# Optimization experiments

Hardware: AMD Instinct MI355X
Metric: run time of the kernel (lower is better)

The kernel has to match this reference:

```python
import jax, jax.numpy as jnp
import numpy as np

B, L, D = 8192, 200, 64
NUM_ITEMS = 100000
HID = 64  # attention hidden_dim


def setup_inputs() -> dict:
    key = jax.random.key(0)
    ks = jax.random.split(key, 16)
    inp = {
        "item_sequence": jax.random.randint(ks[0], (B, L), 0, NUM_ITEMS),
        "click_sequence": jax.random.randint(ks[1], (B, L), 0, 2),
        "seq_length": jax.random.randint(ks[2], (B, 1), 1, L + 1),
        "target_item": jax.random.randint(ks[3], (B, 1), 0, NUM_ITEMS),
        "context_features": jax.random.normal(ks[4], (B, 9), dtype=jnp.float32),
        # embedding table (num_items+1, D)
        "emb_table": jax.random.normal(ks[5], (NUM_ITEMS + 1, D), dtype=jnp.float32) * 0.05,
        # attention MLP: Linear(2D->64), Linear(64->32), Linear(32->1)
        "aw1": jax.random.normal(ks[6], (2 * D, HID), dtype=jnp.float32) * 0.05,
        "ab1": jnp.zeros((HID,), jnp.float32),
        "aw2": jax.random.normal(ks[7], (HID, HID // 2), dtype=jnp.float32) * 0.05,
        "ab2": jnp.zeros((HID // 2,), jnp.float32),
        "aw3": jax.random.normal(ks[8], (HID // 2, 1), dtype=jnp.float32) * 0.05,
        "ab3": jnp.zeros((1,), jnp.float32),
        # context MLP: Linear(9->32)
        "cw": jax.random.normal(ks[9], (9, 32), dtype=jnp.float32) * 0.05,
        "cb": jnp.zeros((32,), jnp.float32),
        # head MLP: Linear(160->128), Linear(128->64), Linear(64->1)
        "mw1": jax.random.normal(ks[10], (2 * D + 32, 128), dtype=jnp.float32) * 0.05,
        "mb1": jnp.zeros((128,), jnp.float32),
        "mw2": jax.random.normal(ks[11], (128, 64), dtype=jnp.float32) * 0.05,
        "mb2": jnp.zeros((64,), jnp.float32),
        "mw3": jax.random.normal(ks[12], (64, 1), dtype=jnp.float32) * 0.05,
        "mb3": jnp.zeros((1,), jnp.float32),
    }
    return inp


def reference(item_sequence, click_sequence, seq_length, target_item, context_features,
              emb_table, aw1, ab1, aw2, ab2, aw3, ab3, cw, cb,
              mw1, mb1, mw2, mb2, mw3, mb3):
    seq_emb = emb_table[item_sequence]                 # [B, L, D]
    tgt_emb = emb_table[target_item[:, 0]]             # [B, D]
    seq_len = item_sequence.shape[1]
    mask = (jnp.arange(seq_len)[None, :] < seq_length).astype(seq_emb.dtype)  # [B, L]

    # DIN attention: concat(query, keys) -> 3-layer MLP -> masked softmax -> weighted sum
    q = jnp.broadcast_to(tgt_emb[:, None, :], seq_emb.shape)          # [B, L, D]
    att_in = jnp.concatenate([q, seq_emb], axis=-1)                   # [B, L, 2D]
    h = jax.nn.relu(att_in @ aw1 + ab1)
    h = jax.nn.relu(h @ aw2 + ab2)
    scores = (h @ aw3 + ab3)[..., 0]                                  # [B, L]
    scores = jnp.where(mask == 0, jnp.asarray(-1e9, scores.dtype), scores)
    w = jax.nn.softmax(scores, axis=1)                                # [B, L]
    attended = jnp.einsum('bl,bld->bd', w, seq_emb)                   # [B, D]

    ctx = jax.nn.relu(context_features @ cw + cb)                     # [B, 32]
    comb = jnp.concatenate([attended, tgt_emb, ctx], axis=1)          # [B, 2D+32]
    h = jax.nn.relu(comb @ mw1 + mb1)
    h = jax.nn.relu(h @ mw2 + mb2)
    out = jax.nn.sigmoid(h @ mw3 + mb3)[:, 0]                         # [B]
    return out
```

## Files before the change

### kernel.cpp

```cpp
#include <hip/hip_runtime.h>
#include <cmath>

typedef __attribute__((ext_vector_type(8))) short s16x8;
typedef __attribute__((ext_vector_type(4))) short s16x4;
typedef __attribute__((ext_vector_type(4))) float f32x4;

__device__ __forceinline__ short f2bf(float f) {
    union { float f; unsigned u; } v; v.f = f;
    unsigned r = v.u + 0x7FFFu + ((v.u >> 16) & 1u);
    return (short)(r >> 16);
}
__device__ __forceinline__ float bf2f(short s) {
    union { unsigned u; float f; } v; v.u = ((unsigned)(unsigned short)s) << 16;
    return v.f;
}
__device__ __forceinline__ s16x8 cvt8(float4 a, float4 b) {
    s16x8 r = { f2bf(a.x), f2bf(a.y), f2bf(a.z), f2bf(a.w),
                f2bf(b.x), f2bf(b.y), f2bf(b.z), f2bf(b.w) };
    return r;
}

#define W1SEQ_SH  0
#define W1TOP_SH  4096
#define W2_SH     8192
#define MW1T_SH   10240
#define MW2T_SH   30720
#define QC_F      19456
#define CB_SH     1087488

__global__ __launch_bounds__(256)
void din_wprep_kernel(const float* __restrict__ aw1,
                      const float* __restrict__ aw2,
                      const float* __restrict__ mw1,
                      const float* __restrict__ mw2,
                      short* __restrict__ ws)
{
    const int wb = blockIdx.x;
    const int t = threadIdx.x;
    if (wb == 0) {
        for (int idx = t; idx < 4096; idx += 256) {
            int j = idx & 7, lane = (idx >> 3) & 63, fr = idx >> 9;
            int n = (fr >> 1) * 16 + (lane & 15);
            int k = (fr & 1) * 32 + (lane >> 4) * 8 + j;
            ws[W1SEQ_SH + idx] = f2bf(aw1[(64 + k) * 64 + n]);
        }
    } else if (wb == 1) {
        for (int idx = t; idx < 4096; idx += 256) {
            int j = idx & 7, lane = (idx >> 3) & 63, fr = idx >> 9;
            int n = (fr >> 1) * 16 + (lane & 15);
            int k = (fr & 1) * 32 + (lane >> 4) * 8 + j;
            ws[W1TOP_SH + idx] = f2bf(aw1[k * 64 + n]);
        }
    } else if (wb == 2) {
        for (int idx = t; idx < 2048; idx += 256) {
            int j = idx & 7, lane = (idx >> 3) & 63, fr = idx >> 9;
            int n = (fr >> 1) * 16 + (lane & 15);
            int k = (fr & 1) * 32 + (lane >> 4) * 8 + j;
            ws[W2_SH + idx] = f2bf(aw2[k * 32 + n]);
        }
    } else if (wb == 3) {
        for (int idx = t; idx < 8192; idx += 256) {
            int j = idx & 7, lane = (idx >> 3) & 63, fr = idx >> 9;
            int n = (fr >> 2) * 16 + (lane & 15);
            int k = (fr & 3) * 32 + (lane >> 4) * 8 + j;
            ws[MW2T_SH + idx] = f2bf(mw2[k * 64 + n]);
        }
    } else {
        const int base = (wb - 4) * 5120;
        for (int ii = t; ii < 5120; ii += 256) {
            int idx = base + ii;
            int j = idx & 7, lane = (idx >> 3) & 63, fr = idx >> 9;
            int nt = fr / 5, ks = fr - nt * 5;
            int n = nt * 16 + (lane & 15);
            int k = ks * 32 + (lane >> 4) * 8 + j;
            ws[MW1T_SH + idx] = f2bf(mw1[k * 128 + n]);
        }
    }
}

__global__ __launch_bounds__(256)
void din_qc_kernel(const int* __restrict__ tgt_item,
                   const float* __restrict__ emb,
                   const float* __restrict__ ab1,
                   short* __restrict__ ws)
{
    const int t = threadIdx.x, lane = t & 63, wave = t >> 6;
    const int quad = lane >> 4, r16 = lane & 15;
    const short* w1t = ws + W1TOP_SH;
    float* qc = (float*)ws + QC_F;

    const int b0 = (blockIdx.x * 4 + wave) * 16;
    const int it = tgt_item[b0 + r16];
    const float* rp = emb + it * 64 + quad * 8;
    float4 v0 = *(const float4*)(rp),      v1 = *(const float4*)(rp + 4);
    float4 v2 = *(const float4*)(rp + 32), v3 = *(const float4*)(rp + 36);
    s16x8 a0 = cvt8(v0, v1);
    s16x8 a1 = cvt8(v2, v3);

    f32x4 acc[4] = {{0,0,0,0},{0,0,0,0},{0,0,0,0},{0,0,0,0}};
    #pragma unroll
    for (int nt = 0; nt < 4; ++nt) {
        s16x8 b_0 = *(const s16x8*)(w1t + ((nt * 2 + 0) * 64 + lane) * 8);
        s16x8 b_1 = *(const s16x8*)(w1t + ((nt * 2 + 1) * 64 + lane) * 8);
        acc[nt] = __builtin_amdgcn_mfma_f32_16x16x32_bf16(a0, b_0, acc[nt], 0, 0, 0);
        acc[nt] = __builtin_amdgcn_mfma_f32_16x16x32_bf16(a1, b_1, acc[nt], 0, 0, 0);
    }
    #pragma unroll
    for (int nt = 0; nt < 4; ++nt) {
        float bias = ab1[nt * 16 + r16];
        #pragma unroll
        for (int rr = 0; rr < 4; ++rr)
            qc[(b0 + quad * 4 + rr) * 64 + nt * 16 + r16] = acc[nt][rr] + bias;
    }
}

#define H1_PITCH 72
__global__ __launch_bounds__(256)
void din_att_v3(const int* __restrict__ item_seq,
                const int* __restrict__ seq_len_p,
                const int* __restrict__ tgt_item,
                const float* __restrict__ ctx_feat,
                const float* __restrict__ emb,
                const float* __restrict__ ab2,
                const float* __restrict__ aw3, const float* __restrict__ ab3,
                const float* __restrict__ cw,  const float* __restrict__ cb,
                short* __restrict__ ws)
{
    const int t = threadIdx.x, lane = t & 63, wave = t >> 6;
    const int quad = lane >> 4, r16 = lane & 15;
    __shared__ short s_w1[4096];
    __shared__ short s_h1[4][16 * H1_PITCH];
    __shared__ float s_sc[4][64];
    __shared__ float s_pool[4][64];
    __shared__ float s_m[4], s_e[4];

    const int b   = blockIdx.x;
    const int len = seq_len_p[b];
    const int tgt = tgt_item[b];

    {
        const s16x8* src = (const s16x8*)(ws + W1SEQ_SH);
        s16x8* dst = (s16x8*)s_w1;
        dst[t]       = src[t];
        dst[t + 256] = src[t + 256];
    }

    bool act[4];
    s16x8 af[4][2];
    #pragma unroll
    for (int ci = 0; ci < 4; ++ci) {
        const int c = wave + ci * 4;
        act[ci] = (c < 13) && (c * 16 < len);
        if (act[ci]) {
            int r = c * 16 + r16; if (r > 199) r = 199;
            const int it = item_seq[b * 200 + r];
            const float* rp = emb + it * 64 + quad * 8;
            float4 v0 = *(const float4*)(rp),      v1 = *(const float4*)(rp + 4);
            float4 v2 = *(const float4*)(rp + 32), v3 = *(const float4*)(rp + 36);
            af[ci][0] = cvt8(v0, v1);
            af[ci][1] = cvt8(v2, v3);
        }
    }
    s16x8 w2r[4];
    #pragma unroll
    for (int fr = 0; fr < 4; ++fr)
        w2r[fr] = *(const s16x8*)(ws + W2_SH + (fr * 64 + lane) * 8);
    const float* qcp = (const float*)ws + QC_F + b * 64;
    float qcv[4];
    #pragma unroll
    for (int nt = 0; nt < 4; ++nt) qcv[nt] = qcp[nt * 16 + r16];
    const float bias2_lo = ab2[r16], bias2_hi = ab2[16 + r16];
    const float w3_lo    = aw3[r16], w3_hi    = aw3[16 + r16];
    const float b3       = ab3[0];
    __syncthreads();

    short* h1w = s_h1[wave];

    #pragma unroll
    for (int ci = 0; ci < 4; ++ci) {
        if (!act[ci]) continue;
        f32x4 acc[4] = {{0,0,0,0},{0,0,0,0},{0,0,0,0},{0,0,0,0}};
        #pragma unroll
        for (int nt = 0; nt < 4; ++nt) {
            s16x8 b_0 = *(const s16x8*)&s_w1[((nt * 2 + 0) * 64 + lane) * 8];
            s16x8 b_1 = *(const s16x8*)&s_w1[((nt * 2 + 1) * 64 + lane) * 8];
            acc[nt] = __builtin_amdgcn_mfma_f32_16x16x32_bf16(af[ci][0], b_0, acc[nt], 0, 0, 0);
            acc[nt] = __builtin_amdgcn_mfma_f32_16x16x32_bf16(af[ci][1], b_1, acc[nt], 0, 0, 0);
        }
        #pragma unroll
        for (int nt = 0; nt < 4; ++nt)
            #pragma unroll
            for (int rr = 0; rr < 4; ++rr) {
                float v = fmaxf(acc[nt][rr] + qcv[nt], 0.f);
                h1w[(quad * 4 + rr) * H1_PITCH + nt * 16 + r16] = f2bf(v);
            }
        __builtin_amdgcn_wave_barrier();

        s16x8 h0  = *(const s16x8*)&h1w[r16 * H1_PITCH + quad * 8];
        s16x8 h1v = *(const s16x8*)&h1w[r16 * H1_PITCH + 32 + quad * 8];
        f32x4 c2[2] = {{0,0,0,0},{0,0,0,0}};
        #pragma unroll
        for (int nt = 0; nt < 2; ++nt) {
            c2[nt] = __builtin_amdgcn_mfma_f32_16x16x32_bf16(h0,  w2r[nt * 2],     c2[nt], 0, 0, 0);
            c2[nt] = __builtin_amdgcn_mfma_f32_16x16x32_bf16(h1v, w2r[nt * 2 + 1], c2[nt], 0, 0, 0);
        }
        #pragma unroll
        for (int rr = 0; rr < 4; ++rr) {
            float p = fmaxf(c2[0][rr] + bias2_lo, 0.f) * w3_lo
                    + fmaxf(c2[1][rr] + bias2_hi, 0.f) * w3_hi;
            p += __shfl_xor(p, 8);
            p += __shfl_xor(p, 4);
            p += __shfl_xor(p, 2);
            p += __shfl_xor(p, 1);
            if (r16 == 0) s_sc[wave][ci * 16 + quad * 4 + rr] = p + b3;
        }
        __builtin_amdgcn_wave_barrier();
    }

    const int ci_l = lane >> 4;
    const int c_l  = wave + ci_l * 4;
    const int grow = c_l * 16 + r16;
    const bool valid = (c_l < 13) && (grow < len);
    float sc = valid ? s_sc[wave][lane] : -1e30f;
    float m = sc;
    #pragma unroll
    for (int off = 32; off; off >>= 1) m = fmaxf(m, __shfl_xor(m, off));
    float e = valid ? __expf(sc - m) : 0.f;
    #pragma unroll
    for (int off = 32; off; off >>= 1) e += __shfl_xor(e, off);

    float p[16];
    #pragma unroll
    for (int i = 0; i < 16; ++i) p[i] = 0.f;
    #pragma unroll
    for (int ci = 0; ci < 4; ++ci) {
        if (!act[ci]) continue;
        const int row = (wave + ci * 4) * 16 + r16;
        const float w = (row < len) ? __expf(s_sc[wave][ci * 16 + r16] - m) : 0.f;
        #pragma unroll
        for (int j = 0; j < 8; ++j) {
            p[j]     += w * bf2f(af[ci][0][j]);
            p[8 + j] += w * bf2f(af[ci][1][j]);
        }
    }
    #pragma unroll
    for (int i = 0; i < 16; ++i) {
        p[i] += __shfl_xor(p[i], 1);
        p[i] += __shfl_xor(p[i], 2);
        p[i] += __shfl_xor(p[i], 4);
        p[i] += __shfl_xor(p[i], 8);
    }
    if (r16 == 0) {
        #pragma unroll
        for (int j = 0; j < 8; ++j) {
            s_pool[wave][quad * 8 + j]      = p[j];
            s_pool[wave][32 + quad * 8 + j] = p[8 + j];
        }
    }
    if (lane == 0) { s_m[wave] = m; s_e[wave] = e; }
    __syncthreads();

    short* comb = ws + CB_SH + b * 160;
    if (t < 64) {
        float gm = fmaxf(fmaxf(s_m[0], s_m[1]), fmaxf(s_m[2], s_m[3]));
        float s0 = __expf(s_m[0] - gm), s1 = __expf(s_m[1] - gm);
        float s2 = __expf(s_m[2] - gm), s3 = __expf(s_m[3] - gm);
        float denom = s0 * s_e[0] + s1 * s_e[1] + s2 * s_e[2] + s3 * s_e[3];
        float pooled = s0 * s_pool[0][t] + s1 * s_pool[1][t]
                     + s2 * s_pool[2][t] + s3 * s_pool[3][t];
        comb[t] = f2bf(pooled / denom);
    } else if (t < 96) {
        const int j = t - 64;
        float a = cb[j];
        #pragma unroll
        for (int k = 0; k < 9; ++k) a += ctx_feat[b * 9 + k] * cw[k * 32 + j];
        comb[128 + j] = f2bf(fmaxf(a, 0.f));
    } else if (t < 160) {
        comb[64 + (t - 96)] = f2bf(emb[tgt * 64 + (t - 96)]);
    }
}

__global__ __launch_bounds__(64)
void din_mlp_kernel(const float* __restrict__ mb1,
                    const float* __restrict__ mb2,
                    const float* __restrict__ mw3, const float* __restrict__ mb3,
                    const short* __restrict__ ws,
                    float* __restrict__ out)
{
    const int lane = threadIdx.x & 63;
    const int quad = lane >> 4, r16 = lane & 15;
    __shared__ short s_h1[16 * 136];
    __shared__ short s_h2[16 * 72];

    const int b0 = blockIdx.x * 16;
    const short* comb = ws + CB_SH;
    const short* w1   = ws + MW1T_SH;
    const short* w2   = ws + MW2T_SH;

    s16x8 a[5];
    #pragma unroll
    for (int ks = 0; ks < 5; ++ks)
        a[ks] = *(const s16x8*)(comb + (b0 + r16) * 160 + ks * 32 + quad * 8);
    f32x4 acc[8] = {{0,0,0,0},{0,0,0,0},{0,0,0,0},{0,0,0,0},{0,0,0,0},{0,0,0,0},{0,0,0,0},{0,0,0,0}};
    #pragma unroll
    for (int nt = 0; nt < 8; ++nt)
        #pragma unroll
        for (int ks = 0; ks < 5; ++ks) {
            s16x8 bf = *(const s16x8*)(w1 + ((nt * 5 + ks) * 64 + lane) * 8);
            acc[nt] = __builtin_amdgcn_mfma_f32_16x16x32_bf16(a[ks], bf, acc[nt], 0, 0, 0);
        }
    #pragma unroll
    for (int nt = 0; nt < 8; ++nt) {
        float bias = mb1[nt * 16 + r16];
        #pragma unroll
        for (int rr = 0; rr < 4; ++rr)
            s_h1[(quad * 4 + rr) * 136 + nt * 16 + r16] = f2bf(fmaxf(acc[nt][rr] + bias, 0.f));
    }
    __builtin_amdgcn_wave_barrier();

    s16x8 a2[4];
    #pragma unroll
    for (int ks = 0; ks < 4; ++ks)
        a2[ks] = *(const s16x8*)&s_h1[r16 * 136 + ks * 32 + quad * 8];
    f32x4 acc2[4] = {{0,0,0,0},{0,0,0,0},{0,0,0,0},{0,0,0,0}};
    #pragma unroll
    for (int nt = 0; nt < 4; ++nt)
        #pragma unroll
        for (int ks = 0; ks < 4; ++ks) {
            s16x8 bf = *(const s16x8*)(w2 + ((nt * 4 + ks) * 64 + lane) * 8);
            acc2[nt] = __builtin_amdgcn_mfma_f32_16x16x32_bf16(a2[ks], bf, acc2[nt], 0, 0, 0);
        }
    #pragma unroll
    for (int nt = 0; nt < 4; ++nt) {
        float bias = mb2[nt * 16 + r16];
        #pragma unroll
        for (int rr = 0; rr < 4; ++rr)
            s_h2[(quad * 4 + rr) * 72 + nt * 16 + r16] = f2bf(fmaxf(acc2[nt][rr] + bias, 0.f));
    }
    __builtin_amdgcn_wave_barrier();

    float p = 0.f;
    #pragma unroll
    for (int j = 0; j < 16; ++j)
        p += bf2f(s_h2[r16 * 72 + quad * 16 + j]) * mw3[quad * 16 + j];
    p += __shfl_xor(p, 16);
    p += __shfl_xor(p, 32);
    if (quad == 0) out[b0 + r16] = 1.f / (1.f + __expf(-(p + mb3[0])));
}

extern "C" void kernel_launch(void* const* d_in, const int* in_sizes, int n_in,
                              void* d_out, int out_size, void* d_ws, size_t ws_size,
                              hipStream_t stream)
{
    const int*   item_seq  = (const int*)  d_in[0];
    const int*   seq_len   = (const int*)  d_in[2];
    const int*   tgt_item  = (const int*)  d_in[3];
    const float* ctx_feat  = (const float*)d_in[4];
    const float* emb       = (const float*)d_in[5];
    const float* aw1 = (const float*)d_in[6];
    const float* ab1 = (const float*)d_in[7];
    const float* aw2 = (const float*)d_in[8];
    const float* ab2 = (const float*)d_in[9];
    const float* aw3 = (const float*)d_in[10];
    const float* ab3 = (const float*)d_in[11];
    const float* cw  = (const float*)d_in[12];
    const float* cb  = (const float*)d_in[13];
    const float* mw1 = (const float*)d_in[14];
    const float* mb1 = (const float*)d_in[15];
    const float* mw2 = (const float*)d_in[16];
    const float* mb2 = (const float*)d_in[17];
    const float* mw3 = (const float*)d_in[18];
    const float* mb3 = (const float*)d_in[19];
    float* out = (float*)d_out;
    short* ws  = (short*)d_ws;

    hipLaunchKernelGGL(din_wprep_kernel, dim3(8), dim3(256), 0, stream,
                       aw1, aw2, mw1, mw2, ws);
    hipLaunchKernelGGL(din_qc_kernel, dim3(128), dim3(256), 0, stream,
                       tgt_item, emb, ab1, ws);
    hipLaunchKernelGGL(din_att_v3, dim3(8192), dim3(256), 0, stream,
                       item_seq, seq_len, tgt_item, ctx_feat, emb,
                       ab2, aw3, ab3, cw, cb, ws);
    hipLaunchKernelGGL(din_mlp_kernel, dim3(512), dim3(64), 0, stream,
                       mb1, mb2, mw3, mb3, ws, out);
}
```

Before: 192.4 us.

## Fuse query projection and head MLP into the per-sample attention kernel

Removes the separate query-projection and head-MLP kernels and computes both inside the per-sample attention kernel. The target projection and head MLP now run per block on MFMA tiles that use only one of sixteen rows, and results stay in shared memory instead of round-tripping through workspace. This saves two launches and the global writes and reads of the qc and comb buffers. In exchange, every block re-reads the head MLP weights and the W1 top weights from global/L2. That multiplies weight traffic about 16x and adds several block-wide barriers.

New measurement: 219.9 us. 14.3% more time.

```diff
diff --git a/kernel.cpp b/kernel.cpp
--- a/kernel.cpp
+++ b/kernel.cpp
@@ -25,8 +25,6 @@
 #define W2_SH     8192
 #define MW1T_SH   10240
 #define MW2T_SH   30720
-#define QC_F      19456
-#define CB_SH     1087488
 
 __global__ __launch_bounds__(256)
 void din_wprep_kernel(const float* __restrict__ aw1,
@@ -78,58 +76,30 @@
     }
 }
 
+#define H1_PITCH 72
 __global__ __launch_bounds__(256)
-void din_qc_kernel(const int* __restrict__ tgt_item,
-                   const float* __restrict__ emb,
-                   const float* __restrict__ ab1,
-                   short* __restrict__ ws)
+void din_one(const int* __restrict__ item_seq,
+             const int* __restrict__ seq_len_p,
+             const int* __restrict__ tgt_item,
+             const float* __restrict__ ctx_feat,
+             const float* __restrict__ emb,
+             const float* __restrict__ ab1,
+             const float* __restrict__ ab2,
+             const float* __restrict__ aw3, const float* __restrict__ ab3,
+             const float* __restrict__ cw,  const float* __restrict__ cb,
+             const float* __restrict__ mb1, const float* __restrict__ mb2,
+             const float* __restrict__ mw3, const float* __restrict__ mb3,
+             const short* __restrict__ ws,
+             float* __restrict__ out)
 {
     const int t = threadIdx.x, lane = t & 63, wave = t >> 6;
     const int quad = lane >> 4, r16 = lane & 15;
-    const short* w1t = ws + W1TOP_SH;
-    float* qc = (float*)ws + QC_F;
-
-    const int b0 = (blockIdx.x * 4 + wave) * 16;
-    const int it = tgt_item[b0 + r16];
-    const float* rp = emb + it * 64 + quad * 8;
-    float4 v0 = *(const float4*)(rp),      v1 = *(const float4*)(rp + 4);
-    float4 v2 = *(const float4*)(rp + 32), v3 = *(const float4*)(rp + 36);
-    s16x8 a0 = cvt8(v0, v1);
-    s16x8 a1 = cvt8(v2, v3);
-
-    f32x4 acc[4] = {{0,0,0,0},{0,0,0,0},{0,0,0,0},{0,0,0,0}};
-    #pragma unroll
-    for (int nt = 0; nt < 4; ++nt) {
-        s16x8 b_0 = *(const s16x8*)(w1t + ((nt * 2 + 0) * 64 + lane) * 8);
-        s16x8 b_1 = *(const s16x8*)(w1t + ((nt * 2 + 1) * 64 + lane) * 8);
-        acc[nt] = __builtin_amdgcn_mfma_f32_16x16x32_bf16(a0, b_0, acc[nt], 0, 0, 0);
-        acc[nt] = __builtin_amdgcn_mfma_f32_16x16x32_bf16(a1, b_1, acc[nt], 0, 0, 0);
-    }
-    #pragma unroll
-    for (int nt = 0; nt < 4; ++nt) {
-        float bias = ab1[nt * 16 + r16];
-        #pragma unroll
-        for (int rr = 0; rr < 4; ++rr)
-            qc[(b0 + quad * 4 + rr) * 64 + nt * 16 + r16] = acc[nt][rr] + bias;
-    }
-}
-
-#define H1_PITCH 72
-__global__ __launch_bounds__(256)
-void din_att_v3(const int* __restrict__ item_seq,
-                const int* __restrict__ seq_len_p,
-                const int* __restrict__ tgt_item,
-                const float* __restrict__ ctx_feat,
-                const float* __restrict__ emb,
-                const float* __restrict__ ab2,
-                const float* __restrict__ aw3, const float* __restrict__ ab3,
-                const float* __restrict__ cw,  const float* __restrict__ cb,
-                short* __restrict__ ws)
-{
-    const int t = threadIdx.x, lane = t & 63, wave = t >> 6;
-    const int quad = lane >> 4, r16 = lane & 15;
-    __shared__ short s_w1[4096];
-    __shared__ short s_h1[4][16 * H1_PITCH];
+    __shared__ __align__(16) short s_w1[4096];
+    __shared__ __align__(16) short s_w2s[2048];
+    __shared__ __align__(16) short s_h1[4][16 * H1_PITCH];
+    __shared__ __align__(16) short s_comb[160];
+    __shared__ __align__(16) short s_hm1[128];
+    __shared__ float s_hm2[64];
     __shared__ float s_sc[4][64];
     __shared__ float s_pool[4][64];
     __shared__ float s_m[4], s_e[4];
@@ -141,9 +111,11 @@
     {
         const s16x8* src = (const s16x8*)(ws + W1SEQ_SH);
         s16x8* dst = (s16x8*)s_w1;
-        dst[t]       = src[t];
-        dst[t + 256] = src[t + 256];
-    }
+        dst[t] = src[t];
+        if (t < 256) ((s16x8*)s_w2s)[t] = ((const s16x8*)(ws + W2_SH))[t];
+        else ((s16x8*)s_w1)[t + 256 - 256 + 256] = src[t + 256 - 256 + 256];
+    }
+    ((s16x8*)s_w1)[t + 256 < 512 ? t + 256 : 511] = ((const s16x8*)(ws + W1SEQ_SH))[t + 256 < 512 ? t + 256 : 511];
 
     bool act[4];
     s16x8 af[4][2];
@@ -161,19 +133,38 @@
             af[ci][1] = cvt8(v2, v3);
         }
     }
-    s16x8 w2r[4];
-    #pragma unroll
-    for (int fr = 0; fr < 4; ++fr)
-        w2r[fr] = *(const s16x8*)(ws + W2_SH + (fr * 64 + lane) * 8);
-    const float* qcp = (const float*)ws + QC_F + b * 64;
+
+    s16x8 at0 = {}, at1 = {};
+    if (r16 == 0) {
+        const float* rp = emb + tgt * 64 + quad * 8;
+        float4 v0 = *(const float4*)(rp),      v1 = *(const float4*)(rp + 4);
+        float4 v2 = *(const float4*)(rp + 32), v3 = *(const float4*)(rp + 36);
+        at0 = cvt8(v0, v1);
+        at1 = cvt8(v2, v3);
+    }
     float qcv[4];
-    #pragma unroll
-    for (int nt = 0; nt < 4; ++nt) qcv[nt] = qcp[nt * 16 + r16];
+    {
+        f32x4 qacc[4] = {{0,0,0,0},{0,0,0,0},{0,0,0,0},{0,0,0,0}};
+        #pragma unroll
+        for (int nt = 0; nt < 4; ++nt) {
+            s16x8 b_0 = *(const s16x8*)(ws + W1TOP_SH + ((nt * 2 + 0) * 64 + lane) * 8);
+            s16x8 b_1 = *(const s16x8*)(ws + W1TOP_SH + ((nt * 2 + 1) * 64 + lane) * 8);
+            qacc[nt] = __builtin_amdgcn_mfma_f32_16x16x32_bf16(at0, b_0, qacc[nt], 0, 0, 0);
+            qacc[nt] = __builtin_amdgcn_mfma_f32_16x16x32_bf16(at1, b_1, qacc[nt], 0, 0, 0);
+        }
+        #pragma unroll
+        for (int nt = 0; nt < 4; ++nt)
+            qcv[nt] = __shfl(qacc[nt][0], r16) + ab1[nt * 16 + r16];
+    }
     const float bias2_lo = ab2[r16], bias2_hi = ab2[16 + r16];
     const float w3_lo    = aw3[r16], w3_hi    = aw3[16 + r16];
     const float b3       = ab3[0];
     __syncthreads();
 
+    s16x8 w2r[4];
+    #pragma unroll
+    for (int fr = 0; fr < 4; ++fr)
+        w2r[fr] = *(const s16x8*)&s_w2s[(fr * 64 + lane) * 8];
     short* h1w = s_h1[wave];
 
     #pragma unroll
@@ -260,7 +251,6 @@
     if (lane == 0) { s_m[wave] = m; s_e[wave] = e; }
     __syncthreads();
 
-    short* comb = ws + CB_SH + b * 160;
     if (t < 64) {
         float gm = fmaxf(fmaxf(s_m[0], s_m[1]), fmaxf(s_m[2], s_m[3]));
         float s0 = __expf(s_m[0] - gm), s1 = __expf(s_m[1] - gm);
@@ -268,84 +258,60 @@
         float denom = s0 * s_e[0] + s1 * s_e[1] + s2 * s_e[2] + s3 * s_e[3];
         float pooled = s0 * s_pool[0][t] + s1 * s_pool[1][t]
                      + s2 * s_pool[2][t] + s3 * s_pool[3][t];
-        comb[t] = f2bf(pooled / denom);
+        s_comb[t] = f2bf(pooled / denom);
     } else if (t < 96) {
         const int j = t - 64;
         float a = cb[j];
         #pragma unroll
         for (int k = 0; k < 9; ++k) a += ctx_feat[b * 9 + k] * cw[k * 32 + j];
-        comb[128 + j] = f2bf(fmaxf(a, 0.f));
+        s_comb[128 + j] = f2bf(fmaxf(a, 0.f));
     } else if (t < 160) {
-        comb[64 + (t - 96)] = f2bf(emb[tgt * 64 + (t - 96)]);
-    }
-}
-
-__global__ __launch_bounds__(64)
-void din_mlp_kernel(const float* __restrict__ mb1,
-                    const float* __restrict__ mb2,
-                    const float* __restrict__ mw3, const float* __restrict__ mb3,
-                    const short* __restrict__ ws,
-                    float* __restrict__ out)
-{
-    const int lane = threadIdx.x & 63;
-    const int quad = lane >> 4, r16 = lane & 15;
-    __shared__ short s_h1[16 * 136];
-    __shared__ short s_h2[16 * 72];
-
-    const int b0 = blockIdx.x * 16;
-    const short* comb = ws + CB_SH;
-    const short* w1   = ws + MW1T_SH;
-    const short* w2   = ws + MW2T_SH;
-
-    s16x8 a[5];
-    #pragma unroll
-    for (int ks = 0; ks < 5; ++ks)
-        a[ks] = *(const s16x8*)(comb + (b0 + r16) * 160 + ks * 32 + quad * 8);
-    f32x4 acc[8] = {{0,0,0,0},{0,0,0,0},{0,0,0,0},{0,0,0,0},{0,0,0,0},{0,0,0,0},{0,0,0,0},{0,0,0,0}};
-    #pragma unroll
-    for (int nt = 0; nt < 8; ++nt)
-        #pragma unroll
-        for (int ks = 0; ks < 5; ++ks) {
-            s16x8 bf = *(const s16x8*)(w1 + ((nt * 5 + ks) * 64 + lane) * 8);
-            acc[nt] = __builtin_amdgcn_mfma_f32_16x16x32_bf16(a[ks], bf, acc[nt], 0, 0, 0);
-        }
-    #pragma unroll
-    for (int nt = 0; nt < 8; ++nt) {
-        float bias = mb1[nt * 16 + r16];
-        #pragma unroll
-        for (int rr = 0; rr < 4; ++rr)
-            s_h1[(quad * 4 + rr) * 136 + nt * 16 + r16] = f2bf(fmaxf(acc[nt][rr] + bias, 0.f));
-    }
-    __builtin_amdgcn_wave_barrier();
-
-    s16x8 a2[4];
-    #pragma unroll
-    for (int ks = 0; ks < 4; ++ks)
-        a2[ks] = *(const s16x8*)&s_h1[r16 * 136 + ks * 32 + quad * 8];
-    f32x4 acc2[4] = {{0,0,0,0},{0,0,0,0},{0,0,0,0},{0,0,0,0}};
-    #pragma unroll
-    for (int nt = 0; nt < 4; ++nt)
+        s_comb[64 + (t - 96)] = f2bf(emb[tgt * 64 + (t - 96)]);
+    }
+    __syncthreads();
+
+    {
+        s16x8 a1f[5];
+        #pragma unroll
+        for (int ks = 0; ks < 5; ++ks)
+            a1f[ks] = *(const s16x8*)&s_comb[ks * 32 + quad * 8];
+        #pragma unroll
+        for (int ni = 0; ni < 2; ++ni) {
+            const int nt = wave * 2 + ni;
+            f32x4 acc = {0, 0, 0, 0};
+            #pragma unroll
+            for (int ks = 0; ks < 5; ++ks) {
+                s16x8 bf = *(const s16x8*)(ws + MW1T_SH + ((nt * 5 + ks) * 64 + lane) * 8);
+                acc = __builtin_amdgcn_mfma_f32_16x16x32_bf16(a1f[ks], bf, acc, 0, 0, 0);
+            }
+            if (quad == 0)
+                s_hm1[nt * 16 + r16] = f2bf(fmaxf(acc[0] + mb1[nt * 16 + r16], 0.f));
+        }
+    }
+    __syncthreads();
+
+    {
+        s16x8 a2f[4];
+        #pragma unroll
+        for (int ks = 0; ks < 4; ++ks)
+            a2f[ks] = *(const s16x8*)&s_hm1[ks * 32 + quad * 8];
+        f32x4 acc = {0, 0, 0, 0};
         #pragma unroll
         for (int ks = 0; ks < 4; ++ks) {
-            s16x8 bf = *(const s16x8*)(w2 + ((nt * 4 + ks) * 64 + lane) * 8);
-            acc2[nt] = __builtin_amdgcn_mfma_f32_16x16x32_bf16(a2[ks], bf, acc2[nt], 0, 0, 0);
-        }
-    #pragma unroll
-    for (int nt = 0; nt < 4; ++nt) {
-        float bias = mb2[nt * 16 + r16];
-        #pragma unroll
-        for (int rr = 0; rr < 4; ++rr)
-            s_h2[(quad * 4 + rr) * 72 + nt * 16 + r16] = f2bf(fmaxf(acc2[nt][rr] + bias, 0.f));
-    }
-    __builtin_amdgcn_wave_barrier();
-
-    float p = 0.f;
-    #pragma unroll
-    for (int j = 0; j < 16; ++j)
-        p += bf2f(s_h2[r16 * 72 + quad * 16 + j]) * mw3[quad * 16 + j];
-    p += __shfl_xor(p, 16);
-    p += __shfl_xor(p, 32);
-    if (quad == 0) out[b0 + r16] = 1.f / (1.f + __expf(-(p + mb3[0])));
+            s16x8 bf = *(const s16x8*)(ws + MW2T_SH + ((wave * 4 + ks) * 64 + lane) * 8);
+            acc = __builtin_amdgcn_mfma_f32_16x16x32_bf16(a2f[ks], bf, acc, 0, 0, 0);
+        }
+        if (quad == 0)
+            s_hm2[wave * 16 + r16] = fmaxf(acc[0] + mb2[wave * 16 + r16], 0.f);
+    }
+    __syncthreads();
+
+    if (t < 64) {
+        float pp = s_hm2[lane] * mw3[lane];
+        #pragma unroll
+        for (int off = 32; off; off >>= 1) pp += __shfl_xor(pp, off);
+        if (lane == 0) out[b] = 1.f / (1.f + __expf(-(pp + mb3[0])));
+    }
 }
 
 extern "C" void kernel_launch(void* const* d_in, const int* in_sizes, int n_in,
@@ -376,11 +342,8 @@
 
     hipLaunchKernelGGL(din_wprep_kernel, dim3(8), dim3(256), 0, stream,
                        aw1, aw2, mw1, mw2, ws);
-    hipLaunchKernelGGL(din_qc_kernel, dim3(128), dim3(256), 0, stream,
-                       tgt_item, emb, ab1, ws);
-    hipLaunchKernelGGL(din_att_v3, dim3(8192), dim3(256), 0, stream,
+    hipLaunchKernelGGL(din_one, dim3(8192), dim3(256), 0, stream,
                        item_seq, seq_len, tgt_item, ctx_feat, emb,
-                       ab2, aw3, ab3, cw, cb, ws);
-    hipLaunchKernelGGL(din_mlp_kernel, dim3(512), dim3(64), 0, stream,
+                       ab1, ab2, aw3, ab3, cw, cb,
                        mb1, mb2, mw3, mb3, ws, out);
 }
```

## Assign one batch row per wave with online softmax and fused query projection

Applied to the files above, without the earlier changes.

The attention kernel now processes one batch element per wave (four per block) instead of one per block. Each wave streams 16-row chunks with an online-softmax running max and sum, and prefetches the next chunk's embeddings while computing the current one. The separate query-projection kernel is removed and its MFMA is computed inline per wave from the target embedding. This drops a launch, the cross-wave reduction and block barrier, and the idle waves seen with short sequences. In exchange each wave's loop is serial over up to 13 chunks, and the w1 copy into shared memory is still done per block.

Measured after the change: 198.3 us. 1.03x slower.

```diff
diff --git a/kernel.cpp b/kernel.cpp
--- a/kernel.cpp
+++ b/kernel.cpp
@@ -25,8 +25,7 @@
 #define W2_SH     8192
 #define MW1T_SH   10240
 #define MW2T_SH   30720
-#define QC_F      19456
-#define CB_SH     1087488
+#define CB_SH     40960
 
 __global__ __launch_bounds__(256)
 void din_wprep_kernel(const float* __restrict__ aw1,
@@ -78,49 +77,14 @@
     }
 }
 
-__global__ __launch_bounds__(256)
-void din_qc_kernel(const int* __restrict__ tgt_item,
-                   const float* __restrict__ emb,
-                   const float* __restrict__ ab1,
-                   short* __restrict__ ws)
-{
-    const int t = threadIdx.x, lane = t & 63, wave = t >> 6;
-    const int quad = lane >> 4, r16 = lane & 15;
-    const short* w1t = ws + W1TOP_SH;
-    float* qc = (float*)ws + QC_F;
-
-    const int b0 = (blockIdx.x * 4 + wave) * 16;
-    const int it = tgt_item[b0 + r16];
-    const float* rp = emb + it * 64 + quad * 8;
-    float4 v0 = *(const float4*)(rp),      v1 = *(const float4*)(rp + 4);
-    float4 v2 = *(const float4*)(rp + 32), v3 = *(const float4*)(rp + 36);
-    s16x8 a0 = cvt8(v0, v1);
-    s16x8 a1 = cvt8(v2, v3);
-
-    f32x4 acc[4] = {{0,0,0,0},{0,0,0,0},{0,0,0,0},{0,0,0,0}};
-    #pragma unroll
-    for (int nt = 0; nt < 4; ++nt) {
-        s16x8 b_0 = *(const s16x8*)(w1t + ((nt * 2 + 0) * 64 + lane) * 8);
-        s16x8 b_1 = *(const s16x8*)(w1t + ((nt * 2 + 1) * 64 + lane) * 8);
-        acc[nt] = __builtin_amdgcn_mfma_f32_16x16x32_bf16(a0, b_0, acc[nt], 0, 0, 0);
-        acc[nt] = __builtin_amdgcn_mfma_f32_16x16x32_bf16(a1, b_1, acc[nt], 0, 0, 0);
-    }
-    #pragma unroll
-    for (int nt = 0; nt < 4; ++nt) {
-        float bias = ab1[nt * 16 + r16];
-        #pragma unroll
-        for (int rr = 0; rr < 4; ++rr)
-            qc[(b0 + quad * 4 + rr) * 64 + nt * 16 + r16] = acc[nt][rr] + bias;
-    }
-}
-
 #define H1_PITCH 72
 __global__ __launch_bounds__(256)
-void din_att_v3(const int* __restrict__ item_seq,
+void din_att_v4(const int* __restrict__ item_seq,
                 const int* __restrict__ seq_len_p,
                 const int* __restrict__ tgt_item,
                 const float* __restrict__ ctx_feat,
                 const float* __restrict__ emb,
+                const float* __restrict__ ab1,
                 const float* __restrict__ ab2,
                 const float* __restrict__ aw3, const float* __restrict__ ab3,
                 const float* __restrict__ cw,  const float* __restrict__ cb,
@@ -128,15 +92,14 @@
 {
     const int t = threadIdx.x, lane = t & 63, wave = t >> 6;
     const int quad = lane >> 4, r16 = lane & 15;
-    __shared__ short s_w1[4096];
-    __shared__ short s_h1[4][16 * H1_PITCH];
-    __shared__ float s_sc[4][64];
-    __shared__ float s_pool[4][64];
-    __shared__ float s_m[4], s_e[4];
-
-    const int b   = blockIdx.x;
+    __shared__ __align__(16) short s_w1[4096];
+    __shared__ __align__(16) short s_h1[4][16 * H1_PITCH];
+    __shared__ float s_scw[4][16];
+
+    const int b   = blockIdx.x * 4 + wave;
     const int len = seq_len_p[b];
     const int tgt = tgt_item[b];
+    const int nc  = (min(len, 200) + 15) >> 4;
 
     {
         const s16x8* src = (const s16x8*)(ws + W1SEQ_SH);
@@ -145,47 +108,69 @@
         dst[t + 256] = src[t + 256];
     }
 
-    bool act[4];
-    s16x8 af[4][2];
-    #pragma unroll
-    for (int ci = 0; ci < 4; ++ci) {
-        const int c = wave + ci * 4;
-        act[ci] = (c < 13) && (c * 16 < len);
-        if (act[ci]) {
-            int r = c * 16 + r16; if (r > 199) r = 199;
-            const int it = item_seq[b * 200 + r];
-            const float* rp = emb + it * 64 + quad * 8;
-            float4 v0 = *(const float4*)(rp),      v1 = *(const float4*)(rp + 4);
-            float4 v2 = *(const float4*)(rp + 32), v3 = *(const float4*)(rp + 36);
-            af[ci][0] = cvt8(v0, v1);
-            af[ci][1] = cvt8(v2, v3);
-        }
+    s16x8 at0 = {}, at1 = {};
+    if (r16 == 0) {
+        const float* rp = emb + tgt * 64 + quad * 8;
+        at0 = cvt8(*(const float4*)(rp),      *(const float4*)(rp + 4));
+        at1 = cvt8(*(const float4*)(rp + 32), *(const float4*)(rp + 36));
+    }
+    float4 nv0, nv1, nv2, nv3;
+    {
+        int r = r16; if (r > len - 1) r = len - 1;
+        const int it = item_seq[b * 200 + r];
+        const float* rp = emb + it * 64 + quad * 8;
+        nv0 = *(const float4*)(rp);      nv1 = *(const float4*)(rp + 4);
+        nv2 = *(const float4*)(rp + 32); nv3 = *(const float4*)(rp + 36);
+    }
+
+    float qcv[4];
+    {
+        f32x4 qacc[4] = {{0,0,0,0},{0,0,0,0},{0,0,0,0},{0,0,0,0}};
+        #pragma unroll
+        for (int nt = 0; nt < 4; ++nt) {
+            s16x8 b_0 = *(const s16x8*)(ws + W1TOP_SH + ((nt * 2 + 0) * 64 + lane) * 8);
+            s16x8 b_1 = *(const s16x8*)(ws + W1TOP_SH + ((nt * 2 + 1) * 64 + lane) * 8);
+            qacc[nt] = __builtin_amdgcn_mfma_f32_16x16x32_bf16(at0, b_0, qacc[nt], 0, 0, 0);
+            qacc[nt] = __builtin_amdgcn_mfma_f32_16x16x32_bf16(at1, b_1, qacc[nt], 0, 0, 0);
+        }
+        #pragma unroll
+        for (int nt = 0; nt < 4; ++nt)
+            qcv[nt] = __shfl(qacc[nt][0], r16) + ab1[nt * 16 + r16];
     }
     s16x8 w2r[4];
     #pragma unroll
     for (int fr = 0; fr < 4; ++fr)
         w2r[fr] = *(const s16x8*)(ws + W2_SH + (fr * 64 + lane) * 8);
-    const float* qcp = (const float*)ws + QC_F + b * 64;
-    float qcv[4];
-    #pragma unroll
-    for (int nt = 0; nt < 4; ++nt) qcv[nt] = qcp[nt * 16 + r16];
     const float bias2_lo = ab2[r16], bias2_hi = ab2[16 + r16];
     const float w3_lo    = aw3[r16], w3_hi    = aw3[16 + r16];
     const float b3       = ab3[0];
     __syncthreads();
 
     short* h1w = s_h1[wave];
-
-    #pragma unroll
-    for (int ci = 0; ci < 4; ++ci) {
-        if (!act[ci]) continue;
+    float* scw = s_scw[wave];
+    float m = -1e30f, e = 0.f;
+    float p[16];
+    #pragma unroll
+    for (int i = 0; i < 16; ++i) p[i] = 0.f;
+
+    for (int c = 0; c < nc; ++c) {
+        s16x8 a0 = cvt8(nv0, nv1);
+        s16x8 a1 = cvt8(nv2, nv3);
+        if (c + 1 < nc) {
+            int r = (c + 1) * 16 + r16; if (r > len - 1) r = len - 1;
+            const int it = item_seq[b * 200 + r];
+            const float* rp = emb + it * 64 + quad * 8;
+            nv0 = *(const float4*)(rp);      nv1 = *(const float4*)(rp + 4);
+            nv2 = *(const float4*)(rp + 32); nv3 = *(const float4*)(rp + 36);
+        }
+
         f32x4 acc[4] = {{0,0,0,0},{0,0,0,0},{0,0,0,0},{0,0,0,0}};
         #pragma unroll
         for (int nt = 0; nt < 4; ++nt) {
             s16x8 b_0 = *(const s16x8*)&s_w1[((nt * 2 + 0) * 64 + lane) * 8];
             s16x8 b_1 = *(const s16x8*)&s_w1[((nt * 2 + 1) * 64 + lane) * 8];
-            acc[nt] = __builtin_amdgcn_mfma_f32_16x16x32_bf16(af[ci][0], b_0, acc[nt], 0, 0, 0);
-            acc[nt] = __builtin_amdgcn_mfma_f32_16x16x32_bf16(af[ci][1], b_1, acc[nt], 0, 0, 0);
+            acc[nt] = __builtin_amdgcn_mfma_f32_16x16x32_bf16(a0, b_0, acc[nt], 0, 0, 0);
+            acc[nt] = __builtin_amdgcn_mfma_f32_16x16x32_bf16(a1, b_1, acc[nt], 0, 0, 0);
         }
         #pragma unroll
         for (int nt = 0; nt < 4; ++nt)
@@ -206,43 +191,40 @@
         }
         #pragma unroll
         for (int rr = 0; rr < 4; ++rr) {
-            float p = fmaxf(c2[0][rr] + bias2_lo, 0.f) * w3_lo
-                    + fmaxf(c2[1][rr] + bias2_hi, 0.f) * w3_hi;
-            p += __shfl_xor(p, 8);
-            p += __shfl_xor(p, 4);
-            p += __shfl_xor(p, 2);
-            p += __shfl_xor(p, 1);
-            if (r16 == 0) s_sc[wave][ci * 16 + quad * 4 + rr] = p + b3;
+            float sco = fmaxf(c2[0][rr] + bias2_lo, 0.f) * w3_lo
+                      + fmaxf(c2[1][rr] + bias2_hi, 0.f) * w3_hi;
+            sco += __shfl_xor(sco, 8);
+            sco += __shfl_xor(sco, 4);
+            sco += __shfl_xor(sco, 2);
+            sco += __shfl_xor(sco, 1);
+            if (r16 == 0) scw[quad * 4 + rr] = sco + b3;
         }
         __builtin_amdgcn_wave_barrier();
-    }
-
-    const int ci_l = lane >> 4;
-    const int c_l  = wave + ci_l * 4;
-    const int grow = c_l * 16 + r16;
-    const bool valid = (c_l < 13) && (grow < len);
-    float sc = valid ? s_sc[wave][lane] : -1e30f;
-    float m = sc;
-    #pragma unroll
-    for (int off = 32; off; off >>= 1) m = fmaxf(m, __shfl_xor(m, off));
-    float e = valid ? __expf(sc - m) : 0.f;
-    #pragma unroll
-    for (int off = 32; off; off >>= 1) e += __shfl_xor(e, off);
-
-    float p[16];
-    #pragma unroll
-    for (int i = 0; i < 16; ++i) p[i] = 0.f;
-    #pragma unroll
-    for (int ci = 0; ci < 4; ++ci) {
-        if (!act[ci]) continue;
-        const int row = (wave + ci * 4) * 16 + r16;
-        const float w = (row < len) ? __expf(s_sc[wave][ci * 16 + r16] - m) : 0.f;
+
+        float sc = scw[r16];
+        if (c * 16 + r16 >= len) sc = -1e30f;
+        float cm = sc;
+        cm = fmaxf(cm, __shfl_xor(cm, 1));
+        cm = fmaxf(cm, __shfl_xor(cm, 2));
+        cm = fmaxf(cm, __shfl_xor(cm, 4));
+        cm = fmaxf(cm, __shfl_xor(cm, 8));
+        const float mn = fmaxf(m, cm);
+        const float alpha = __expf(m - mn);
+        const float w = __expf(sc - mn);
+        float wsum = w;
+        wsum += __shfl_xor(wsum, 1);
+        wsum += __shfl_xor(wsum, 2);
+        wsum += __shfl_xor(wsum, 4);
+        wsum += __shfl_xor(wsum, 8);
+        e = e * alpha + wsum;
+        m = mn;
         #pragma unroll
         for (int j = 0; j < 8; ++j) {
-            p[j]     += w * bf2f(af[ci][0][j]);
-            p[8 + j] += w * bf2f(af[ci][1][j]);
-        }
-    }
+            p[j]     = p[j]     * alpha + w * bf2f(a0[j]);
+            p[8 + j] = p[8 + j] * alpha + w * bf2f(a1[j]);
+        }
+    }
+
     #pragma unroll
     for (int i = 0; i < 16; ++i) {
         p[i] += __shfl_xor(p[i], 1);
@@ -250,33 +232,21 @@
         p[i] += __shfl_xor(p[i], 4);
         p[i] += __shfl_xor(p[i], 8);
     }
+    short* comb = ws + CB_SH + b * 160;
+    const float inv = 1.f / e;
     if (r16 == 0) {
         #pragma unroll
         for (int j = 0; j < 8; ++j) {
-            s_pool[wave][quad * 8 + j]      = p[j];
-            s_pool[wave][32 + quad * 8 + j] = p[8 + j];
-        }
-    }
-    if (lane == 0) { s_m[wave] = m; s_e[wave] = e; }
-    __syncthreads();
-
-    short* comb = ws + CB_SH + b * 160;
-    if (t < 64) {
-        float gm = fmaxf(fmaxf(s_m[0], s_m[1]), fmaxf(s_m[2], s_m[3]));
-        float s0 = __expf(s_m[0] - gm), s1 = __expf(s_m[1] - gm);
-        float s2 = __expf(s_m[2] - gm), s3 = __expf(s_m[3] - gm);
-        float denom = s0 * s_e[0] + s1 * s_e[1] + s2 * s_e[2] + s3 * s_e[3];
-        float pooled = s0 * s_pool[0][t] + s1 * s_pool[1][t]
-                     + s2 * s_pool[2][t] + s3 * s_pool[3][t];
-        comb[t] = f2bf(pooled / denom);
-    } else if (t < 96) {
-        const int j = t - 64;
-        float a = cb[j];
-        #pragma unroll
-        for (int k = 0; k < 9; ++k) a += ctx_feat[b * 9 + k] * cw[k * 32 + j];
-        comb[128 + j] = f2bf(fmaxf(a, 0.f));
-    } else if (t < 160) {
-        comb[64 + (t - 96)] = f2bf(emb[tgt * 64 + (t - 96)]);
+            comb[quad * 8 + j]      = f2bf(p[j] * inv);
+            comb[32 + quad * 8 + j] = f2bf(p[8 + j] * inv);
+        }
+    }
+    comb[64 + lane] = f2bf(emb[tgt * 64 + lane]);
+    if (lane < 32) {
+        float a = cb[lane];
+        #pragma unroll
+        for (int k = 0; k < 9; ++k) a += ctx_feat[b * 9 + k] * cw[k * 32 + lane];
+        comb[128 + lane] = f2bf(fmaxf(a, 0.f));
     }
 }
 
@@ -376,11 +346,9 @@
 
     hipLaunchKernelGGL(din_wprep_kernel, dim3(8), dim3(256), 0, stream,
                        aw1, aw2, mw1, mw2, ws);
-    hipLaunchKernelGGL(din_qc_kernel, dim3(128), dim3(256), 0, stream,
-                       tgt_item, emb, ab1, ws);
-    hipLaunchKernelGGL(din_att_v3, dim3(8192), dim3(256), 0, stream,
+    hipLaunchKernelGGL(din_att_v4, dim3(2048), dim3(256), 0, stream,
                        item_seq, seq_len, tgt_item, ctx_feat, emb,
-                       ab2, aw3, ab3, cw, cb, ws);
+                       ab1, ab2, aw3, ab3, cw, cb, ws);
     hipLaunchKernelGGL(din_mlp_kernel, dim3(512), dim3(64), 0, stream,
                        mb1, mb2, mw3, mb3, ws, out);
 }
```
